# Kernel tuning notes

Hardware: AMD Instinct MI355X
Metric: run time of the kernel (lower is better)

Reference implementation:

```python
import jax, jax.numpy as jnp
import numpy as np

WS = 8  # window size
NH = 8  # num heads
LN_EPS = 1e-5


def _rel_pos_index(ws):
    coords = np.stack(np.meshgrid(np.arange(ws), np.arange(ws), indexing='ij'))  # [2,ws,ws]
    cf = coords.reshape(2, -1)                      # [2, ws*ws]
    rc = (cf[:, :, None] - cf[:, None, :]).transpose(1, 2, 0).astype(np.int64)  # [N,N,2]
    rc[..., 0] += ws - 1
    rc[..., 1] += ws - 1
    rc[..., 0] *= 2 * ws - 1
    return jnp.asarray(rc.sum(-1), dtype=jnp.int32)  # [N,N]


def setup_inputs() -> dict:
    key = jax.random.key(0)
    B, C, H, W = 8, 256, 128, 128
    hid = 4 * C
    ks = jax.random.split(key, 16)
    rn = lambda k, shape, s=0.02: (jax.random.normal(k, shape, jnp.float32) * s)
    return {
        'x': jax.random.normal(ks[0], (B, H * W, C), jnp.float32),
        'feature': jax.random.normal(ks[1], (B, C, H, W), jnp.float32),
        'Wq': rn(ks[2], (C, C)), 'bq': jnp.zeros((C,), jnp.float32),
        'Wk': rn(ks[3], (C, C)), 'bk': jnp.zeros((C,), jnp.float32),
        'Wv': rn(ks[4], (C, C)), 'bv': jnp.zeros((C,), jnp.float32),
        'Wo': rn(ks[5], (C, C)), 'bo': jnp.zeros((C,), jnp.float32),
        'rpb_table': rn(ks[6], ((2 * WS - 1) ** 2, NH)),
        'g1': jnp.ones((C,), jnp.float32), 'beta1': jnp.zeros((C,), jnp.float32),
        'g2': jnp.ones((C,), jnp.float32), 'beta2': jnp.zeros((C,), jnp.float32),
        'Wm1': rn(ks[7], (C, hid)), 'bm1': jnp.zeros((hid,), jnp.float32),
        'Wm2': rn(ks[8], (hid, C)), 'bm2': jnp.zeros((C,), jnp.float32),
        'Wu1': rn(ks[9], (C, C)), 'bu1': jnp.zeros((C,), jnp.float32),
        'Wu2': rn(ks[10], (C, C)), 'bu2': jnp.zeros((C,), jnp.float32),
        'rel_idx': _rel_pos_index(WS),
    }


def _gelu(t):
    return jax.nn.gelu(t, approximate=False)  # torch nn.GELU default (erf)


def _ln(t, g, b):
    mu = jnp.mean(t, axis=-1, keepdims=True)
    var = jnp.var(t, axis=-1, keepdims=True)
    return (t - mu) * jax.lax.rsqrt(var + LN_EPS) * g + b


def reference(x, feature, Wq, bq, Wk, bk, Wv, bv, Wo, bo, rpb_table,
              g1, beta1, g2, beta2, Wm1, bm1, Wm2, bm2, Wu1, bu1, Wu2, bu2,
              rel_idx):
    B, C, H, W = feature.shape
    ws, nh = WS, NH
    hd = C // nh
    scale = hd ** -0.5

    # unary potential: Linear -> GELU -> Linear on x [B, HW, C]
    unary = _gelu(x @ Wu1 + bu1) @ Wu2 + bu2

    # window partition of feature
    f = feature.reshape(B, C, H * W).transpose(0, 2, 1)  # [B, HW, C]
    pad_h = (-H) % ws
    pad_w = (-W) % ws
    fimg = f.reshape(B, H, W, C)
    if pad_h or pad_w:
        fimg = jnp.pad(fimg, ((0, 0), (0, pad_h), (0, pad_w), (0, 0)))
    Hp, Wp_ = H + pad_h, W + pad_w
    win = fimg.reshape(B, Hp // ws, ws, Wp_ // ws, ws, C)
    win = win.transpose(0, 1, 3, 2, 4, 5).reshape(-1, ws * ws, C)  # [nW, N, C]

    xn = _ln(win, g1, beta1)
    N = ws * ws
    q = (xn @ Wq + bq).reshape(-1, N, nh, hd).transpose(0, 2, 1, 3)  # [nW, h, N, d]
    k = (xn @ Wk + bk).reshape(-1, N, nh, hd).transpose(0, 2, 1, 3)
    v = (xn @ Wv + bv).reshape(-1, N, nh, hd).transpose(0, 2, 1, 3)

    attn = jnp.einsum('whnd,whmd->whnm', q, k) * scale
    bias = rpb_table[rel_idx.reshape(-1)].reshape(N, N, nh).transpose(2, 0, 1)  # [h,N,N]
    attn = jax.nn.softmax(attn + bias[None], axis=-1)
    o = jnp.einsum('whnm,whmd->whnd', attn, v)
    o = o.transpose(0, 2, 1, 3).reshape(-1, N, C) @ Wo + bo  # [nW, N, C]

    # window reverse
    rev = o.reshape(B, Hp // ws, Wp_ // ws, ws, ws, C)
    rev = rev.transpose(0, 1, 3, 2, 4, 5).reshape(B, Hp, Wp_, C)
    if pad_h or pad_w:
        rev = rev[:, :H, :W, :]
    rev = rev.reshape(B, H * W, C)

    x2 = unary + rev
    out = x2 + (_gelu(_ln(x2, g2, beta2) @ Wm1 + bm1) @ Wm2 + bm2)
    return out
```

## Files before the change

kernel.cpp:

```cpp
#include <hip/hip_runtime.h>
#include <cmath>


typedef unsigned short u16;
typedef unsigned int u32;
typedef __bf16 bf16x8 __attribute__((ext_vector_type(8)));
typedef float f32x4 __attribute__((ext_vector_type(4)));

#define EPI_NONE 0
#define EPI_GELU 1
#define EPI_WINREV 2
#define EPI_ADD 3

#define MTOK 131072
#define CC 256
#define HWC 16384

__device__ __forceinline__ float b2f(u16 u) {
    union { u32 i; float f; } x; x.i = ((u32)u) << 16; return x.f;
}
__device__ __forceinline__ u16 f2b(float f) {
    union { float f; u32 i; } x; x.f = f;
    u32 r = x.i + 0x7fffu + ((x.i >> 16) & 1u);
    return (u16)(r >> 16);
}
__device__ __forceinline__ u32 cvtpk(float lo, float hi) {
    u32 r;
    asm("v_cvt_pk_bf16_f32 %0, %1, %2" : "=v"(r) : "v"(lo), "v"(hi));
    return r;
}
__device__ __forceinline__ float gelu_f(float v) {
    return 0.5f * v * (1.0f + erff(v * 0.7071067811865475f));
}

__global__ __launch_bounds__(256) void cvt_f32_bf16(
    const float* __restrict__ src, u16* __restrict__ dst, long n)
{
    long i = ((long)blockIdx.x * 256 + threadIdx.x) * 8;
    if (i >= n) return;
    float4 a = *(const float4*)(src + i);
    float4 b = *(const float4*)(src + i + 4);
    union { uint4 v; u16 u[8]; } o;
    o.u[0] = f2b(a.x); o.u[1] = f2b(a.y); o.u[2] = f2b(a.z); o.u[3] = f2b(a.w);
    o.u[4] = f2b(b.x); o.u[5] = f2b(b.y); o.u[6] = f2b(b.z); o.u[7] = f2b(b.w);
    *(uint4*)(dst + i) = o.v;
}

__global__ __launch_bounds__(256) void transpose_f32_bf16(
    const float* __restrict__ src, u16* __restrict__ dst, int K, int N)
{
    __shared__ float t[32][33];
    const int k0 = blockIdx.x * 32, n0 = blockIdx.y * 32;
    const int tx = threadIdx.x & 31, ty = threadIdx.x >> 5;
    for (int i = ty; i < 32; i += 8)
        t[i][tx] = src[(long)(k0 + i) * N + n0 + tx];
    __syncthreads();
    for (int i = ty; i < 32; i += 8)
        dst[(long)(n0 + i) * K + k0 + tx] = f2b(t[tx][i]);
}

__global__ __launch_bounds__(256) void rpb_gather(
    const float* __restrict__ rpb, const int* __restrict__ rel, float* __restrict__ outb)
{
    int e = blockIdx.x * 256 + threadIdx.x;
    int h = e >> 12, idx = e & 4095;
    int mi = idx >> 10, ni = (idx >> 8) & 3, lane = (idx >> 2) & 63, r = idx & 3;
    int row = mi * 16 + (lane >> 4) * 4 + r;
    int tok = 4 * (lane & 15) + ni;
    outb[e] = 1.4426950408889634f * rpb[rel[row * 64 + tok] * 8 + h];
}

__global__ __launch_bounds__(256) void win_ln(
    const float* __restrict__ feat, const float* __restrict__ g1,
    const float* __restrict__ be1, u16* __restrict__ xn)
{
    __shared__ u16 tile[256 * 65];
    __shared__ float red1[256];
    __shared__ float red2[256];
    __shared__ float mu_s[64];
    __shared__ float rs_s[64];
    const int wid = blockIdx.x;
    const int bI = wid >> 8, rem = wid & 255, wh = rem >> 4, ww = rem & 15;
    const int c = threadIdx.x;
    const float* fp = feat + ((long)(bI * CC + c)) * HWC + (wh * 8) * 128 + ww * 8;
#pragma unroll
    for (int i = 0; i < 8; i++) {
        float4 a = *(const float4*)(fp + i * 128);
        float4 b = *(const float4*)(fp + i * 128 + 4);
        tile[c * 65 + i * 8 + 0] = f2b(a.x);
        tile[c * 65 + i * 8 + 1] = f2b(a.y);
        tile[c * 65 + i * 8 + 2] = f2b(a.z);
        tile[c * 65 + i * 8 + 3] = f2b(a.w);
        tile[c * 65 + i * 8 + 4] = f2b(b.x);
        tile[c * 65 + i * 8 + 5] = f2b(b.y);
        tile[c * 65 + i * 8 + 6] = f2b(b.z);
        tile[c * 65 + i * 8 + 7] = f2b(b.w);
    }
    __syncthreads();
    {
        const int n = threadIdx.x & 63, p = threadIdx.x >> 6;
        float s1 = 0.f, s2 = 0.f;
        for (int j = 0; j < 64; j++) {
            float v = b2f(tile[(p * 64 + j) * 65 + n]);
            s1 += v; s2 += v * v;
        }
        red1[n * 4 + p] = s1; red2[n * 4 + p] = s2;
    }
    __syncthreads();
    if (threadIdx.x < 64) {
        int t = threadIdx.x;
        float a = red1[t * 4] + red1[t * 4 + 1] + red1[t * 4 + 2] + red1[t * 4 + 3];
        float b = red2[t * 4] + red2[t * 4 + 1] + red2[t * 4 + 2] + red2[t * 4 + 3];
        float mu = a * (1.f / 256.f);
        float var = b * (1.f / 256.f) - mu * mu;
        mu_s[t] = mu;
        rs_s[t] = rsqrtf(var + 1e-5f);
    }
    __syncthreads();
    const float gc = g1[c], bc = be1[c];
    u16* xp = xn + (long)wid * 64 * 256 + c;
    for (int n2 = 0; n2 < 64; n2++) {
        float v = (b2f(tile[c * 65 + n2]) - mu_s[n2]) * rs_s[n2] * gc + bc;
        xp[n2 * 256] = f2b(v);
    }
}

__global__ __launch_bounds__(256) void ln_rows(
    const u16* __restrict__ x, const float* __restrict__ g2,
    const float* __restrict__ be2, u16* __restrict__ out)
{
    const int wave = threadIdx.x >> 6, lane = threadIdx.x & 63;
    const long row = (long)blockIdx.x * 4 + wave;
    union { uint2 v; u16 u[4]; } pk;
    pk.v = *(const uint2*)(x + row * 256 + lane * 4);
    float v0 = b2f(pk.u[0]), v1 = b2f(pk.u[1]), v2 = b2f(pk.u[2]), v3 = b2f(pk.u[3]);
    float s1 = v0 + v1 + v2 + v3;
    float s2 = v0 * v0 + v1 * v1 + v2 * v2 + v3 * v3;
    for (int off = 1; off < 64; off <<= 1) {
        s1 += __shfl_xor(s1, off);
        s2 += __shfl_xor(s2, off);
    }
    float mu = s1 * (1.f / 256.f);
    float var = s2 * (1.f / 256.f) - mu * mu;
    float rs = rsqrtf(var + 1e-5f);
    float4 go = *(const float4*)(g2 + lane * 4);
    float4 bo2 = *(const float4*)(be2 + lane * 4);
    union { uint2 v; u16 u[4]; } ot;
    ot.u[0] = f2b((v0 - mu) * rs * go.x + bo2.x);
    ot.u[1] = f2b((v1 - mu) * rs * go.y + bo2.y);
    ot.u[2] = f2b((v2 - mu) * rs * go.z + bo2.z);
    ot.u[3] = f2b((v3 - mu) * rs * go.w + bo2.w);
    *(uint2*)(out + row * 256 + lane * 4) = ot.v;
}

template <int EPI, bool OUTF32>
__global__ __launch_bounds__(256) void gemm_bt(
    const u16* __restrict__ A, const u16* __restrict__ BT,
    const float* __restrict__ bias, void* __restrict__ outv,
    const u16* __restrict__ res, int M, int N, int K)
{
    __shared__ u16 As[128 * 32];
    __shared__ u16 Bs[128 * 32];
    const int tid = threadIdx.x;
    const int m0 = blockIdx.x * 128;
    const int n0 = blockIdx.y * 128;
    const int wave = tid >> 6, lane = tid & 63;
    const int wm = wave >> 1, wn = wave & 1;
    const int quad = lane >> 4, l16 = lane & 15;

    f32x4 acc[4][4];
#pragma unroll
    for (int i = 0; i < 4; i++)
#pragma unroll
        for (int j = 0; j < 4; j++) acc[i][j] = (f32x4){0.f, 0.f, 0.f, 0.f};

    const int srow = wave * 32 + (lane >> 2);
    const int scol = (lane & 3) * 8;
    const u16* gA = A + (long)(m0 + srow) * K + scol;
    const u16* gB = BT + (long)(n0 + srow) * K + scol;
    u16* lA = &As[srow * 32 + scol];
    u16* lB = &Bs[srow * 32 + scol];

    for (int k0 = 0; k0 < K; k0 += 32) {
        __syncthreads();
        __builtin_amdgcn_global_load_lds(
            (const __attribute__((address_space(1))) void*)(gA + k0),
            (__attribute__((address_space(3))) void*)lA, 16, 0, 0);
        __builtin_amdgcn_global_load_lds(
            (const __attribute__((address_space(1))) void*)(gA + k0 + 16 * K),
            (__attribute__((address_space(3))) void*)(lA + 16 * 32), 16, 0, 0);
        __builtin_amdgcn_global_load_lds(
            (const __attribute__((address_space(1))) void*)(gB + k0),
            (__attribute__((address_space(3))) void*)lB, 16, 0, 0);
        __builtin_amdgcn_global_load_lds(
            (const __attribute__((address_space(1))) void*)(gB + k0 + 16 * K),
            (__attribute__((address_space(3))) void*)(lB + 16 * 32), 16, 0, 0);
        __syncthreads();
        bf16x8 af[4], bfr[4];
#pragma unroll
        for (int mi = 0; mi < 4; mi++)
            af[mi] = *(const bf16x8*)&As[(wm * 64 + mi * 16 + l16) * 32 + quad * 8];
#pragma unroll
        for (int ni = 0; ni < 4; ni++)
            bfr[ni] = *(const bf16x8*)&Bs[(wn * 64 + ni * 16 + l16) * 32 + quad * 8];
#pragma unroll
        for (int mi = 0; mi < 4; mi++)
#pragma unroll
            for (int ni = 0; ni < 4; ni++)
                acc[mi][ni] = __builtin_amdgcn_mfma_f32_16x16x32_bf16(
                    af[mi], bfr[ni], acc[mi][ni], 0, 0, 0);
    }

    float bv[4];
#pragma unroll
    for (int ni = 0; ni < 4; ni++) bv[ni] = bias[n0 + wn * 64 + ni * 16 + l16];

#pragma unroll
    for (int mi = 0; mi < 4; mi++) {
#pragma unroll
        for (int r = 0; r < 4; r++) {
            int row = m0 + wm * 64 + mi * 16 + quad * 4 + r;
            long orow;
            if constexpr (EPI == EPI_WINREV) {
                int wI = row >> 6, n = row & 63;
                int bI = wI >> 8, rem = wI & 255;
                int wh = rem >> 4, wwI = rem & 15;
                orow = (long)bI * HWC + (long)((wh * 8 + (n >> 3)) * 128 + wwI * 8 + (n & 7));
            } else {
                orow = row;
            }
#pragma unroll
            for (int ni = 0; ni < 4; ni++) {
                int col = n0 + wn * 64 + ni * 16 + l16;
                float v = acc[mi][ni][r] + bv[ni];
                if constexpr (EPI == EPI_GELU) v = gelu_f(v);
                if constexpr (EPI == EPI_WINREV || EPI == EPI_ADD)
                    v += b2f(res[orow * (long)N + col]);
                if constexpr (OUTF32)
                    ((float*)outv)[orow * (long)N + col] = v;
                else
                    ((u16*)outv)[orow * (long)N + col] = f2b(v);
            }
        }
    }
}

__global__ __launch_bounds__(256, 3) void attn_kernel(
    const u16* __restrict__ qb, const u16* __restrict__ kb,
    const u16* __restrict__ vb, const float* __restrict__ biasp,
    u16* __restrict__ ob)
{
    __shared__ u16 lds[4 * 6400];
    const int wave = threadIdx.x >> 6, lane = threadIdx.x & 63;
    const int quad = lane >> 4, l16 = lane & 15;
    const int w = blockIdx.x >> 1;
    const int h = ((blockIdx.x & 1) << 2) + wave;
    u16* Pl = lds + wave * 6400;
    u16* VT = Pl + 4096;
    const long base = (long)w * 64 * 256 + h * 32;

    bf16x8 aq[4], bk4[4];
#pragma unroll
    for (int mi = 0; mi < 4; mi++)
        aq[mi] = *(const bf16x8*)(qb + base + (long)(mi * 16 + l16) * 256 + quad * 8);
#pragma unroll
    for (int ni = 0; ni < 4; ni++)
        bk4[ni] = *(const bf16x8*)(kb + base + (long)(4 * l16 + ni) * 256 + quad * 8);

    {
        const int t = lane;
        const int s = ((t >> 4) & 1) * 32 + ((t >> 2) & 3) * 8 + (t >> 5) * 4 + (t & 3);
        const u16* vp = vb + base + (long)t * 256;
        union { uint4 v; u16 u[8]; } p0, p1, p2, p3;
        p0.v = *(const uint4*)(vp);
        p1.v = *(const uint4*)(vp + 8);
        p2.v = *(const uint4*)(vp + 16);
        p3.v = *(const uint4*)(vp + 24);
#pragma unroll
        for (int j = 0; j < 8; j++) {
            VT[j * 72 + s]        = p0.u[j];
            VT[(8 + j) * 72 + s]  = p1.u[j];
            VT[(16 + j) * 72 + s] = p2.u[j];
            VT[(24 + j) * 72 + s] = p3.u[j];
        }
    }

    f32x4 s[4][4];
#pragma unroll
    for (int i = 0; i < 4; i++)
#pragma unroll
        for (int j = 0; j < 4; j++) s[i][j] = (f32x4){0.f, 0.f, 0.f, 0.f};
    __builtin_amdgcn_s_setprio(1);
#pragma unroll
    for (int mi = 0; mi < 4; mi++)
#pragma unroll
        for (int ni = 0; ni < 4; ni++)
            s[mi][ni] = __builtin_amdgcn_mfma_f32_16x16x32_bf16(aq[mi], bk4[ni], s[mi][ni], 0, 0, 0);
    __builtin_amdgcn_s_setprio(0);

    const float* bp = biasp + h * 4096;
    const float SC2 = 0.17677669529663687f * 1.4426950408889634f;
    const int pq = l16 & 3, pks = (l16 >> 2) & 1, ph = l16 >> 3;
#pragma unroll
    for (int mi = 0; mi < 4; mi++) {
        f32x4 bb[4];
#pragma unroll
        for (int ni = 0; ni < 4; ni++)
            bb[ni] = *(const f32x4*)(bp + ((mi * 4 + ni) << 8) + lane * 4);
#pragma unroll
        for (int r = 0; r < 4; r++) {
            float p[4];
#pragma unroll
            for (int ni = 0; ni < 4; ni++)
                p[ni] = __builtin_amdgcn_exp2f(s[mi][ni][r] * SC2 + bb[ni][r]);
            float sum = (p[0] + p[1]) + (p[2] + p[3]);
            for (int off = 1; off < 16; off <<= 1) sum += __shfl_xor(sum, off);
            float inv = __builtin_amdgcn_rcpf(sum);
            int mrow = mi * 16 + quad * 4 + r;
            uint2 w2;
            w2.x = cvtpk(p[0] * inv, p[1] * inv);
            w2.y = cvtpk(p[2] * inv, p[3] * inv);
            *(uint2*)&Pl[pks * 2048 + mrow * 32 + pq * 8 + ph * 4] = w2;
        }
    }

    f32x4 o4[2][4];
#pragma unroll
    for (int i = 0; i < 2; i++)
#pragma unroll
        for (int j = 0; j < 4; j++) o4[i][j] = (f32x4){0.f, 0.f, 0.f, 0.f};
#pragma unroll
    for (int ks = 0; ks < 2; ks++) {
        bf16x8 at[2], pb[4];
#pragma unroll
        for (int mi = 0; mi < 2; mi++)
            at[mi] = *(const bf16x8*)&VT[(mi * 16 + l16) * 72 + ks * 32 + quad * 8];
#pragma unroll
        for (int nt = 0; nt < 4; nt++)
            pb[nt] = *(const bf16x8*)&Pl[ks * 2048 + (nt * 16 + l16) * 32 + quad * 8];
        __builtin_amdgcn_s_setprio(1);
#pragma unroll
        for (int mi = 0; mi < 2; mi++)
#pragma unroll
            for (int nt = 0; nt < 4; nt++)
                o4[mi][nt] = __builtin_amdgcn_mfma_f32_16x16x32_bf16(at[mi], pb[nt], o4[mi][nt], 0, 0, 0);
        __builtin_amdgcn_s_setprio(0);
    }

#pragma unroll
    for (int nt = 0; nt < 4; nt++)
#pragma unroll
        for (int mi = 0; mi < 2; mi++) {
            uint2 w2;
            w2.x = cvtpk(o4[mi][nt][0], o4[mi][nt][1]);
            w2.y = cvtpk(o4[mi][nt][2], o4[mi][nt][3]);
            *(uint2*)(ob + base + (long)(nt * 16 + l16) * 256 + mi * 16 + quad * 4) = w2;
        }
}

extern "C" void kernel_launch(void* const* d_in, const int* in_sizes, int n_in,
                              void* d_out, int out_size, void* d_ws, size_t ws_size,
                              hipStream_t stream)
{
    (void)in_sizes; (void)n_in; (void)out_size; (void)ws_size;
    const float* x    = (const float*)d_in[0];
    const float* feat = (const float*)d_in[1];
    const float* Wq = (const float*)d_in[2];   const float* bq = (const float*)d_in[3];
    const float* Wk = (const float*)d_in[4];   const float* bk = (const float*)d_in[5];
    const float* Wv = (const float*)d_in[6];   const float* bv = (const float*)d_in[7];
    const float* Wo = (const float*)d_in[8];   const float* bo = (const float*)d_in[9];
    const float* rpb = (const float*)d_in[10];
    const float* g1 = (const float*)d_in[11];  const float* be1 = (const float*)d_in[12];
    const float* g2 = (const float*)d_in[13];  const float* be2 = (const float*)d_in[14];
    const float* Wm1 = (const float*)d_in[15]; const float* bm1 = (const float*)d_in[16];
    const float* Wm2 = (const float*)d_in[17]; const float* bm2 = (const float*)d_in[18];
    const float* Wu1 = (const float*)d_in[19]; const float* bu1 = (const float*)d_in[20];
    const float* Wu2 = (const float*)d_in[21]; const float* bu2 = (const float*)d_in[22];
    const int* rel = (const int*)d_in[23];
    float* outp = (float*)d_out;

    char* ws = (char*)d_ws;
    u16* WqT  = (u16*)(ws);
    u16* WkT  = WqT + 65536;
    u16* WvT  = WkT + 65536;
    u16* WoT  = WvT + 65536;
    u16* Wu1T = WoT + 65536;
    u16* Wu2T = Wu1T + 65536;
    u16* Wm1T = Wu2T + 65536;
    u16* Wm2T = Wm1T + 262144;
    float* biasf = (float*)(ws + 1835008);
    const long MB = 1024L * 1024;
    u16* S0 = (u16*)(ws + 2 * MB);
    u16* S1 = (u16*)(ws + 66 * MB);
    u16* S2 = (u16*)(ws + 130 * MB);
    u16* xn  = (u16*)d_out;
    u16* qb  = S0;
    u16* kb  = S1;
    u16* vb  = S2;
    u16* O   = S0;
    u16* xb  = S1;
    u16* u1h = S2;
    u16* un  = S1;
    u16* x2  = S2;
    u16* tch = S0;
    u16* hch = S1;

    const dim3 blk(256);

    transpose_f32_bf16<<<dim3(8, 8), blk, 0, stream>>>(Wq, WqT, 256, 256);
    transpose_f32_bf16<<<dim3(8, 8), blk, 0, stream>>>(Wk, WkT, 256, 256);
    transpose_f32_bf16<<<dim3(8, 8), blk, 0, stream>>>(Wv, WvT, 256, 256);
    transpose_f32_bf16<<<dim3(8, 8), blk, 0, stream>>>(Wo, WoT, 256, 256);
    transpose_f32_bf16<<<dim3(8, 8), blk, 0, stream>>>(Wu1, Wu1T, 256, 256);
    transpose_f32_bf16<<<dim3(8, 8), blk, 0, stream>>>(Wu2, Wu2T, 256, 256);
    transpose_f32_bf16<<<dim3(8, 32), blk, 0, stream>>>(Wm1, Wm1T, 256, 1024);
    transpose_f32_bf16<<<dim3(32, 8), blk, 0, stream>>>(Wm2, Wm2T, 1024, 256);
    rpb_gather<<<dim3(128), blk, 0, stream>>>(rpb, rel, biasf);

    win_ln<<<dim3(2048), blk, 0, stream>>>(feat, g1, be1, xn);

    gemm_bt<EPI_NONE, false><<<dim3(1024, 2), blk, 0, stream>>>(xn, WqT, bq, qb, nullptr, MTOK, 256, 256);
    gemm_bt<EPI_NONE, false><<<dim3(1024, 2), blk, 0, stream>>>(xn, WkT, bk, kb, nullptr, MTOK, 256, 256);
    gemm_bt<EPI_NONE, false><<<dim3(1024, 2), blk, 0, stream>>>(xn, WvT, bv, vb, nullptr, MTOK, 256, 256);

    attn_kernel<<<dim3(4096), blk, 0, stream>>>(qb, kb, vb, biasf, O);

    cvt_f32_bf16<<<dim3(16384), blk, 0, stream>>>(x, xb, (long)MTOK * 256);
    gemm_bt<EPI_GELU, false><<<dim3(1024, 2), blk, 0, stream>>>(xb, Wu1T, bu1, u1h, nullptr, MTOK, 256, 256);
    gemm_bt<EPI_NONE, false><<<dim3(1024, 2), blk, 0, stream>>>(u1h, Wu2T, bu2, un, nullptr, MTOK, 256, 256);

    gemm_bt<EPI_WINREV, false><<<dim3(1024, 2), blk, 0, stream>>>(O, WoT, bo, x2, un, MTOK, 256, 256);

    for (int ch = 0; ch < 4; ch++) {
        const u16* x2c = x2 + (long)ch * 32768 * 256;
        float* outc = outp + (long)ch * 32768 * 256;
        ln_rows<<<dim3(8192), blk, 0, stream>>>(x2c, g2, be2, tch);
        gemm_bt<EPI_GELU, false><<<dim3(256, 8), blk, 0, stream>>>(tch, Wm1T, bm1, hch, nullptr, 32768, 1024, 256);
        gemm_bt<EPI_ADD, true><<<dim3(256, 2), blk, 0, stream>>>(hch, Wm2T, bm2, outc, x2c, 32768, 256, 1024);
    }
}
```

Baseline: 1.087 ms.

## Keep tokens in image order; window-gather in attention, vectorize GEMM epilogue

```diff
diff --git a/kernel.cpp b/kernel.cpp
--- a/kernel.cpp
+++ b/kernel.cpp
@@ -9,7 +9,6 @@
 
 #define EPI_NONE 0
 #define EPI_GELU 1
-#define EPI_WINREV 2
 #define EPI_ADD 3
 
 #define MTOK 131072
@@ -70,58 +69,87 @@
     outb[e] = 1.4426950408889634f * rpb[rel[row * 64 + tok] * 8 + h];
 }
 
-__global__ __launch_bounds__(256) void win_ln(
-    const float* __restrict__ feat, const float* __restrict__ g1,
+__global__ __launch_bounds__(256) void ln_stats(
+    const float* __restrict__ feat, float* __restrict__ muP, float* __restrict__ rsP)
+{
+    __shared__ float red1[4][256];
+    __shared__ float red2[4][256];
+    const int blk = blockIdx.x;
+    const int b = blk >> 6, h2 = blk & 63;
+    const int t = threadIdx.x;
+    const int c_off = t >> 6, lane = t & 63;
+    const int rl = lane >> 5, w4 = (lane & 31) * 4;
+    const int tok0 = rl * 128 + w4;
+    const float* fp = feat + (long)b * 256 * HWC + (long)(h2 * 2 + rl) * 128 + w4;
+    float s1[4] = {0.f, 0.f, 0.f, 0.f};
+    float s2[4] = {0.f, 0.f, 0.f, 0.f};
+#pragma unroll 4
+    for (int it = 0; it < 64; it++) {
+        int c = it * 4 + c_off;
+        float4 f = *(const float4*)(fp + (long)c * HWC);
+        s1[0] += f.x; s2[0] += f.x * f.x;
+        s1[1] += f.y; s2[1] += f.y * f.y;
+        s1[2] += f.z; s2[2] += f.z * f.z;
+        s1[3] += f.w; s2[3] += f.w * f.w;
+    }
+    *(float4*)&red1[c_off][tok0] = *(float4*)s1;
+    *(float4*)&red2[c_off][tok0] = *(float4*)s2;
+    __syncthreads();
+    float a = red1[0][t] + red1[1][t] + red1[2][t] + red1[3][t];
+    float q = red2[0][t] + red2[1][t] + red2[2][t] + red2[3][t];
+    float mu = a * (1.f / 256.f);
+    float var = q * (1.f / 256.f) - mu * mu;
+    long tg = (long)b * HWC + h2 * 256 + t;
+    muP[tg] = mu;
+    rsP[tg] = rsqrtf(var + 1e-5f);
+}
+
+__global__ __launch_bounds__(256) void ln_transpose(
+    const float* __restrict__ feat, const float* __restrict__ muP,
+    const float* __restrict__ rsP, const float* __restrict__ g1,
     const float* __restrict__ be1, u16* __restrict__ xn)
 {
-    __shared__ u16 tile[256 * 65];
-    __shared__ float red1[256];
-    __shared__ float red2[256];
-    __shared__ float mu_s[64];
-    __shared__ float rs_s[64];
-    const int wid = blockIdx.x;
-    const int bI = wid >> 8, rem = wid & 255, wh = rem >> 4, ww = rem & 15;
-    const int c = threadIdx.x;
-    const float* fp = feat + ((long)(bI * CC + c)) * HWC + (wh * 8) * 128 + ww * 8;
-#pragma unroll
-    for (int i = 0; i < 8; i++) {
-        float4 a = *(const float4*)(fp + i * 128);
-        float4 b = *(const float4*)(fp + i * 128 + 4);
-        tile[c * 65 + i * 8 + 0] = f2b(a.x);
-        tile[c * 65 + i * 8 + 1] = f2b(a.y);
-        tile[c * 65 + i * 8 + 2] = f2b(a.z);
-        tile[c * 65 + i * 8 + 3] = f2b(a.w);
-        tile[c * 65 + i * 8 + 4] = f2b(b.x);
-        tile[c * 65 + i * 8 + 5] = f2b(b.y);
-        tile[c * 65 + i * 8 + 6] = f2b(b.z);
-        tile[c * 65 + i * 8 + 7] = f2b(b.w);
-    }
-    __syncthreads();
-    {
-        const int n = threadIdx.x & 63, p = threadIdx.x >> 6;
-        float s1 = 0.f, s2 = 0.f;
-        for (int j = 0; j < 64; j++) {
-            float v = b2f(tile[(p * 64 + j) * 65 + n]);
-            s1 += v; s2 += v * v;
-        }
-        red1[n * 4 + p] = s1; red2[n * 4 + p] = s2;
-    }
-    __syncthreads();
-    if (threadIdx.x < 64) {
-        int t = threadIdx.x;
-        float a = red1[t * 4] + red1[t * 4 + 1] + red1[t * 4 + 2] + red1[t * 4 + 3];
-        float b = red2[t * 4] + red2[t * 4 + 1] + red2[t * 4 + 2] + red2[t * 4 + 3];
-        float mu = a * (1.f / 256.f);
-        float var = b * (1.f / 256.f) - mu * mu;
-        mu_s[t] = mu;
-        rs_s[t] = rsqrtf(var + 1e-5f);
-    }
-    __syncthreads();
-    const float gc = g1[c], bc = be1[c];
-    u16* xp = xn + (long)wid * 64 * 256 + c;
-    for (int n2 = 0; n2 < 64; n2++) {
-        float v = (b2f(tile[c * 65 + n2]) - mu_s[n2]) * rs_s[n2] * gc + bc;
-        xp[n2 * 256] = f2b(v);
+    __shared__ u16 ct[64 * 258];
+    const int blk = blockIdx.x;
+    const int b = blk >> 6, h2 = blk & 63;
+    const int t = threadIdx.x;
+    const int c_off = t >> 6, lane = t & 63;
+    const int rl = lane >> 5, w4 = (lane & 31) * 4;
+    const int tok0 = rl * 128 + w4;
+    const long tokg0 = (long)b * HWC + h2 * 256;
+    const float4 mu4 = *(const float4*)(muP + tokg0 + tok0);
+    const float4 rs4 = *(const float4*)(rsP + tokg0 + tok0);
+    const float* fp = feat + (long)b * 256 * HWC + (long)(h2 * 2 + rl) * 128 + w4;
+    const int koff = t & 3;
+
+    for (int ch = 0; ch < 4; ch++) {
+#pragma unroll
+        for (int it = 0; it < 16; it++) {
+            int c = ch * 64 + it * 4 + c_off;
+            float4 f = *(const float4*)(fp + (long)c * HWC);
+            float gg = g1[c], bb = be1[c];
+            float v0 = (f.x - mu4.x) * rs4.x * gg + bb;
+            float v1 = (f.y - mu4.y) * rs4.y * gg + bb;
+            float v2 = (f.z - mu4.z) * rs4.z * gg + bb;
+            float v3 = (f.w - mu4.w) * rs4.w * gg + bb;
+            uint2 pk;
+            pk.x = cvtpk(v0, v1);
+            pk.y = cvtpk(v2, v3);
+            *(uint2*)&ct[(it * 4 + c_off) * 258 + tok0] = pk;
+        }
+        __syncthreads();
+#pragma unroll
+        for (int p = 0; p < 4; p++) {
+            int token = p * 64 + (t >> 2);
+            union { uint4 q[2]; u16 u[16]; } pkk;
+#pragma unroll
+            for (int cc = 0; cc < 16; cc++)
+                pkk.u[cc] = ct[(koff * 16 + cc) * 258 + token];
+            u16* op = xn + (tokg0 + token) * 256 + ch * 64 + koff * 16;
+            *(uint4*)(op) = pkk.q[0];
+            *(uint4*)(op + 8) = pkk.q[1];
+        }
+        __syncthreads();
     }
 }
 
@@ -208,41 +236,47 @@
 #pragma unroll
             for (int ni = 0; ni < 4; ni++)
                 acc[mi][ni] = __builtin_amdgcn_mfma_f32_16x16x32_bf16(
-                    af[mi], bfr[ni], acc[mi][ni], 0, 0, 0);
-    }
-
-    float bv[4];
-#pragma unroll
-    for (int ni = 0; ni < 4; ni++) bv[ni] = bias[n0 + wn * 64 + ni * 16 + l16];
+                    bfr[ni], af[mi], acc[mi][ni], 0, 0, 0);
+    }
 
 #pragma unroll
     for (int mi = 0; mi < 4; mi++) {
-#pragma unroll
-        for (int r = 0; r < 4; r++) {
-            int row = m0 + wm * 64 + mi * 16 + quad * 4 + r;
-            long orow;
-            if constexpr (EPI == EPI_WINREV) {
-                int wI = row >> 6, n = row & 63;
-                int bI = wI >> 8, rem = wI & 255;
-                int wh = rem >> 4, wwI = rem & 15;
-                orow = (long)bI * HWC + (long)((wh * 8 + (n >> 3)) * 128 + wwI * 8 + (n & 7));
+        const int row = m0 + wm * 64 + mi * 16 + l16;
+        const long rb = (long)row * N;
+#pragma unroll
+        for (int ni = 0; ni < 4; ni++) {
+            const int cb = n0 + wn * 64 + ni * 16 + quad * 4;
+            float4 bb = *(const float4*)(bias + cb);
+            float v0 = acc[mi][ni][0] + bb.x;
+            float v1 = acc[mi][ni][1] + bb.y;
+            float v2 = acc[mi][ni][2] + bb.z;
+            float v3 = acc[mi][ni][3] + bb.w;
+            if constexpr (EPI == EPI_GELU) {
+                v0 = gelu_f(v0); v1 = gelu_f(v1);
+                v2 = gelu_f(v2); v3 = gelu_f(v3);
+            }
+            if constexpr (EPI == EPI_ADD) {
+                uint2 rr = *(const uint2*)(res + rb + cb);
+                v0 += b2f((u16)(rr.x & 0xffff));
+                v1 += b2f((u16)(rr.x >> 16));
+                v2 += b2f((u16)(rr.y & 0xffff));
+                v3 += b2f((u16)(rr.y >> 16));
+            }
+            if constexpr (OUTF32) {
+                float4 o = {v0, v1, v2, v3};
+                *(float4*)((float*)outv + rb + cb) = o;
             } else {
-                orow = row;
+                uint2 o;
+                o.x = cvtpk(v0, v1);
+                o.y = cvtpk(v2, v3);
+                *(uint2*)((u16*)outv + rb + cb) = o;
             }
-#pragma unroll
-            for (int ni = 0; ni < 4; ni++) {
-                int col = n0 + wn * 64 + ni * 16 + l16;
-                float v = acc[mi][ni][r] + bv[ni];
-                if constexpr (EPI == EPI_GELU) v = gelu_f(v);
-                if constexpr (EPI == EPI_WINREV || EPI == EPI_ADD)
-                    v += b2f(res[orow * (long)N + col]);
-                if constexpr (OUTF32)
-                    ((float*)outv)[orow * (long)N + col] = v;
-                else
-                    ((u16*)outv)[orow * (long)N + col] = f2b(v);
-            }
-        }
-    }
+        }
+    }
+}
+
+__device__ __forceinline__ long toff(int n) {
+    return (long)((n >> 3) * 32768 + (n & 7) * 256);
 }
 
 __global__ __launch_bounds__(256, 3) void attn_kernel(
@@ -253,24 +287,25 @@
     __shared__ u16 lds[4 * 6400];
     const int wave = threadIdx.x >> 6, lane = threadIdx.x & 63;
     const int quad = lane >> 4, l16 = lane & 15;
-    const int w = blockIdx.x >> 1;
+    const int wid = blockIdx.x >> 1;
     const int h = ((blockIdx.x & 1) << 2) + wave;
+    const int bI = wid >> 8, wh = (wid >> 4) & 15, ww = wid & 15;
     u16* Pl = lds + wave * 6400;
     u16* VT = Pl + 4096;
-    const long base = (long)w * 64 * 256 + h * 32;
+    const long base = ((long)bI * HWC + (wh * 8) * 128 + ww * 8) * 256 + h * 32;
 
     bf16x8 aq[4], bk4[4];
 #pragma unroll
     for (int mi = 0; mi < 4; mi++)
-        aq[mi] = *(const bf16x8*)(qb + base + (long)(mi * 16 + l16) * 256 + quad * 8);
+        aq[mi] = *(const bf16x8*)(qb + base + toff(mi * 16 + l16) + quad * 8);
 #pragma unroll
     for (int ni = 0; ni < 4; ni++)
-        bk4[ni] = *(const bf16x8*)(kb + base + (long)(4 * l16 + ni) * 256 + quad * 8);
+        bk4[ni] = *(const bf16x8*)(kb + base + toff(4 * l16 + ni) + quad * 8);
 
     {
         const int t = lane;
         const int s = ((t >> 4) & 1) * 32 + ((t >> 2) & 3) * 8 + (t >> 5) * 4 + (t & 3);
-        const u16* vp = vb + base + (long)t * 256;
+        const u16* vp = vb + base + toff(t);
         union { uint4 v; u16 u[8]; } p0, p1, p2, p3;
         p0.v = *(const uint4*)(vp);
         p1.v = *(const uint4*)(vp + 8);
@@ -354,7 +389,7 @@
             uint2 w2;
             w2.x = cvtpk(o4[mi][nt][0], o4[mi][nt][1]);
             w2.y = cvtpk(o4[mi][nt][2], o4[mi][nt][3]);
-            *(uint2*)(ob + base + (long)(nt * 16 + l16) * 256 + mi * 16 + quad * 4) = w2;
+            *(uint2*)(ob + base + toff(nt * 16 + l16) + mi * 16 + quad * 4) = w2;
         }
 }
 
@@ -394,6 +429,8 @@
     u16* S1 = (u16*)(ws + 66 * MB);
     u16* S2 = (u16*)(ws + 130 * MB);
     u16* xn  = (u16*)d_out;
+    float* muP = (float*)((char*)d_out + 96 * MB);
+    float* rsP = (float*)((char*)d_out + 97 * MB);
     u16* qb  = S0;
     u16* kb  = S1;
     u16* vb  = S2;
@@ -417,7 +454,8 @@
     transpose_f32_bf16<<<dim3(32, 8), blk, 0, stream>>>(Wm2, Wm2T, 1024, 256);
     rpb_gather<<<dim3(128), blk, 0, stream>>>(rpb, rel, biasf);
 
-    win_ln<<<dim3(2048), blk, 0, stream>>>(feat, g1, be1, xn);
+    ln_stats<<<dim3(512), blk, 0, stream>>>(feat, muP, rsP);
+    ln_transpose<<<dim3(512), blk, 0, stream>>>(feat, muP, rsP, g1, be1, xn);
 
     gemm_bt<EPI_NONE, false><<<dim3(1024, 2), blk, 0, stream>>>(xn, WqT, bq, qb, nullptr, MTOK, 256, 256);
     gemm_bt<EPI_NONE, false><<<dim3(1024, 2), blk, 0, stream>>>(xn, WkT, bk, kb, nullptr, MTOK, 256, 256);
@@ -429,7 +467,7 @@
     gemm_bt<EPI_GELU, false><<<dim3(1024, 2), blk, 0, stream>>>(xb, Wu1T, bu1, u1h, nullptr, MTOK, 256, 256);
     gemm_bt<EPI_NONE, false><<<dim3(1024, 2), blk, 0, stream>>>(u1h, Wu2T, bu2, un, nullptr, MTOK, 256, 256);
 
-    gemm_bt<EPI_WINREV, false><<<dim3(1024, 2), blk, 0, stream>>>(O, WoT, bo, x2, un, MTOK, 256, 256);
+    gemm_bt<EPI_ADD, false><<<dim3(1024, 2), blk, 0, stream>>>(O, WoT, bo, x2, un, MTOK, 256, 256);
 
     for (int ch = 0; ch < 4; ch++) {
         const u16* x2c = x2 + (long)ch * 32768 * 256;
```

After: 1.123 ms. 1.03x slower.
